# Performance work log

Measured on AMD Instinct MI355X. Metric: run time of the kernel, lower is better.

Reference implementation:

```python
import jax, jax.numpy as jnp
import numpy as np

# MSDeformAttn-style fusion config (canonical deformable-DETR defaults)
D = 256      # d_model
NH = 8       # n_heads
NP = 4       # n_points per level
NL = 2       # n_levels (= num_feature_levels: modality v and modality i)
B, H, W = 4, 64, 64


def setup_inputs() -> dict:
    key = jax.random.key(0)
    ks = jax.random.split(key, 8)
    s = 0.02
    return {
        'input_v': jax.random.normal(ks[0], (B, D, H, W), jnp.float32),
        'input_i': jax.random.normal(ks[1], (B, D, H, W), jnp.float32),
        'W_value': jax.random.normal(ks[2], (D, D), jnp.float32) * s,
        'b_value': jnp.zeros((D,), jnp.float32),
        'W_off':   jax.random.normal(ks[3], (D, NH * NL * NP * 2), jnp.float32) * s,
        'b_off':   jax.random.normal(ks[4], (NH * NL * NP * 2,), jnp.float32) * s,
        'W_attn':  jax.random.normal(ks[5], (D, NH * NL * NP), jnp.float32) * s,
        'b_attn':  jnp.zeros((NH * NL * NP,), jnp.float32),
        'W_out':   jax.random.normal(ks[6], (D, D), jnp.float32) * s,
        'b_out':   jnp.zeros((D,), jnp.float32),
    }


def _bilinear_sample(value_l, locs, Hl, Wl):
    # value_l: (B, NH, HW, dh)  flattened per-level value
    # locs:    (B, Lq, NH, NP, 2) normalized sampling locations in [0,1]
    # returns  (B, NH, Lq, NP, dh); grid_sample semantics: zeros padding, align_corners=False
    b, nh, hw, dh = value_l.shape
    lq = locs.shape[1]
    x = locs[..., 0] * Wl - 0.5
    y = locs[..., 1] * Hl - 0.5
    x0 = jnp.floor(x)
    y0 = jnp.floor(y)
    dx = x - x0
    dy = y - y0
    x0i = x0.astype(jnp.int32)
    y0i = y0.astype(jnp.int32)
    out = jnp.zeros((b, nh, lq, NP, dh), value_l.dtype)
    corners = [
        (x0i,     y0i,     (1 - dx) * (1 - dy)),
        (x0i + 1, y0i,     dx * (1 - dy)),
        (x0i,     y0i + 1, (1 - dx) * dy),
        (x0i + 1, y0i + 1, dx * dy),
    ]
    for xi, yi, wgt in corners:
        valid = ((xi >= 0) & (xi < Wl) & (yi >= 0) & (yi < Hl)).astype(value_l.dtype)
        idx = jnp.clip(yi, 0, Hl - 1) * Wl + jnp.clip(xi, 0, Wl - 1)      # (B,Lq,NH,NP)
        idx_t = idx.transpose(0, 2, 1, 3).reshape(b, nh, lq * NP, 1)       # (B,NH,Lq*NP,1)
        g = jnp.take_along_axis(value_l, idx_t, axis=2)                    # (B,NH,Lq*NP,dh)
        g = g.reshape(b, nh, lq, NP, dh)
        w_t = (wgt * valid).transpose(0, 2, 1, 3)[..., None]               # (B,NH,Lq,NP,1)
        out = out + g * w_t
    return out


def reference(input_v, input_i, W_value, b_value, W_off, b_off, W_attn, b_attn, W_out, b_out):
    b, c, h, w = input_v.shape
    hw = h * w
    lq = NL * hw
    dh = c // NH

    # flatten both modalities into one token sequence (level 0 = v, level 1 = i)
    src_v = input_v.reshape(b, c, hw).transpose(0, 2, 1)
    src_i = input_i.reshape(b, c, hw).transpose(0, 2, 1)
    src = jnp.concatenate([src_v, src_i], axis=1)                          # (B, Lq, C)

    value = (src @ W_value + b_value).reshape(b, lq, NH, dh)
    value = value.transpose(0, 2, 1, 3)                                    # (B, NH, Lq, dh)
    value_levels = [value[:, :, :hw], value[:, :, hw:]]

    offsets = (src @ W_off + b_off).reshape(b, lq, NH, NL, NP, 2)
    attn = jax.nn.softmax((src @ W_attn + b_attn).reshape(b, lq, NH, NL * NP), axis=-1)
    attn = attn.reshape(b, lq, NH, NL, NP)

    # reference points: normalized pixel centers, same grid for both levels
    xs = (jnp.arange(w, dtype=jnp.float32) + 0.5) / w
    ys = (jnp.arange(h, dtype=jnp.float32) + 0.5) / h
    gy, gx = jnp.meshgrid(ys, xs, indexing='ij')
    ref = jnp.stack([gx.reshape(-1), gy.reshape(-1)], axis=-1)             # (HW, 2)
    ref = jnp.concatenate([ref, ref], axis=0)                              # (Lq, 2)

    norm = jnp.array([w, h], dtype=jnp.float32)
    locs = ref[None, :, None, None, None, :] + offsets / norm              # (B,Lq,NH,NL,NP,2)

    sampled = jnp.stack(
        [_bilinear_sample(value_levels[l], locs[:, :, :, l], h, w) for l in range(NL)],
        axis=3)                                                            # (B,NH,Lq,NL,NP,dh)

    fused = jnp.einsum('bqhlp,bhqlpd->bqhd', attn, sampled).reshape(b, lq, c)
    out = fused @ W_out + b_out                                            # (B, Lq, C)

    out_v = out[:, :hw]
    out_i = out[:, hw:]
    o = out_v + out_i                                                      # (B, HW, C)
    return o.transpose(0, 2, 1).reshape(b, c, h, w)
```

## Files before the change

### kernel.cpp

```cpp
#include <hip/hip_runtime.h>

#define HW 4096
#define LQ 8192
#define DD 256

typedef __bf16 bf16x8 __attribute__((ext_vector_type(8)));
typedef float  f32x4  __attribute__((ext_vector_type(4)));
typedef unsigned int u32;
typedef u32 u32x4 __attribute__((ext_vector_type(4)));

#define GLOAD16(g, l) __builtin_amdgcn_global_load_lds(                     \
    (__attribute__((address_space(1))) void*)(g),                          \
    (__attribute__((address_space(3))) void*)(l), 16, 0, 0)

__global__ __launch_bounds__(256) void prep_src(const float* __restrict__ in_v,
                                                const float* __restrict__ in_i,
                                                char* __restrict__ srcS)
{
    __shared__ float tile[64][68];
    const int q0 = blockIdx.x * 64;
    const int k0 = blockIdx.y * 64;
    const int bz = blockIdx.z;
    const float* src = ((bz & 1) ? in_i : in_v) + (size_t)(bz >> 1) * (DD * HW);
    const int t  = threadIdx.x;
    const int ql = (t & 15) * 4;
    const int kl = t >> 4;
#pragma unroll
    for (int rr = 0; rr < 4; ++rr) {
        const float4 v = *(const float4*)(src + (size_t)(k0 + kl + rr * 16) * HW + q0 + ql);
        *(float4*)&tile[kl + rr * 16][ql] = v;
    }
    __syncthreads();
    const int qrow = t >> 2;
    const int kc   = (t & 3) * 16;
    const int row  = (bz >> 1) * LQ + (bz & 1) * HW + q0 + qrow;
    bf16x8 p0, p1;
#pragma unroll
    for (int j = 0; j < 8; ++j) {
        p0[j] = (__bf16)tile[kc + j][qrow];
        p1[j] = (__bf16)tile[kc + 8 + j][qrow];
    }
    char* drow = srcS + (size_t)row * 512;
    const int sw   = (row & 7) << 4;
    const int base = k0 * 2 + kc * 2;
    *(bf16x8*)(drow + ((base)      ^ sw)) = p0;
    *(bf16x8*)(drow + ((base + 16) ^ sw)) = p1;
}

__global__ __launch_bounds__(256) void prep_w(const float* __restrict__ Wv,
                                              const float* __restrict__ Wo,
                                              const float* __restrict__ Wa,
                                              const float* __restrict__ Wout,
                                              char* __restrict__ WcatT,
                                              char* __restrict__ WoutT)
{
    const int gi = blockIdx.x * 256 + threadIdx.x;
    if (gi < 448 * 32) {
        const int row = gi >> 5;
        const int g   = gi & 31;
        const int k   = g * 8;
        const float* col; int stride;
        if (row < 256)      { col = Wv + row;         stride = 256; }
        else if (row < 384) { col = Wo + (row - 256); stride = 128; }
        else                { col = Wa + (row - 384); stride = 64;  }
        bf16x8 p;
#pragma unroll
        for (int j = 0; j < 8; ++j) p[j] = (__bf16)col[(size_t)(k + j) * stride];
        char* d = WcatT + (size_t)row * 512;
        *(bf16x8*)(d + ((g * 16) ^ ((row & 7) << 4))) = p;
    } else {
        const int gj = gi - 448 * 32;
        if (gj >= 256 * 64) return;
        const int c = gj >> 6;
        const int g = gj & 63;
        const int k = (g * 8) & 255;
        bf16x8 p;
#pragma unroll
        for (int j = 0; j < 8; ++j) p[j] = (__bf16)Wout[(size_t)(k + j) * 256 + c];
        char* d = WoutT + (size_t)c * 1024;
        *(bf16x8*)(d + ((g * 16) ^ ((c & 7) << 4))) = p;
    }
}

__global__ __launch_bounds__(256) void mfma_proj(const char* __restrict__ srcS,
                                                 const char* __restrict__ WcatT,
                                                 const float* __restrict__ b_value,
                                                 const float* __restrict__ b_off,
                                                 const float* __restrict__ b_attn,
                                                 __bf16* __restrict__ valueB,
                                                 float* __restrict__ off,
                                                 float* __restrict__ attn)
{
    __shared__ char smem[24576];
    char* As = smem;
    char* Bs = smem + 16384;

    const int M0 = blockIdx.x * 128;
    const int N0 = blockIdx.y * 64;
    const int t = threadIdx.x;
    const int w = t >> 6;
    const int l = t & 63;
    const int lm = l & 15, lk = l >> 4;
    const int wave_m = (w >> 1) * 64;
    const int wave_n = (w & 1) * 32;

    f32x4 acc[4][2] = {};

    const char* Ab = As + (wave_m + lm) * 128;
    const char* Bb = Bs + (wave_n + lm) * 128;
    const int go0 = (lk ^ (l & 7)) * 16;
    const int go1 = go0 ^ 64;

    for (int kt = 0; kt < 4; ++kt) {
        __syncthreads();
        const int kb = kt * 128;
#pragma unroll
        for (int c = 0; c < 4; ++c) {
            const char* g = srcS + (size_t)(M0 + w * 32 + c * 8 + (l >> 3)) * 512 + kb + (l & 7) * 16;
            GLOAD16(g, As + (w * 4 + c) * 1024);
        }
#pragma unroll
        for (int c = 0; c < 2; ++c) {
            const char* g = WcatT + (size_t)(N0 + w * 16 + c * 8 + (l >> 3)) * 512 + kb + (l & 7) * 16;
            GLOAD16(g, Bs + (w * 2 + c) * 1024);
        }
        __syncthreads();

        bf16x8 af[4], bb[2];
#pragma unroll
        for (int mi = 0; mi < 4; ++mi) af[mi] = *(const bf16x8*)(Ab + mi * 2048 + go0);
#pragma unroll
        for (int ni = 0; ni < 2; ++ni) bb[ni] = *(const bf16x8*)(Bb + ni * 2048 + go0);
#pragma unroll
        for (int mi = 0; mi < 4; ++mi)
#pragma unroll
            for (int ni = 0; ni < 2; ++ni)
                acc[mi][ni] = __builtin_amdgcn_mfma_f32_16x16x32_bf16(af[mi], bb[ni], acc[mi][ni], 0, 0, 0);
#pragma unroll
        for (int mi = 0; mi < 4; ++mi) af[mi] = *(const bf16x8*)(Ab + mi * 2048 + go1);
#pragma unroll
        for (int ni = 0; ni < 2; ++ni) bb[ni] = *(const bf16x8*)(Bb + ni * 2048 + go1);
#pragma unroll
        for (int mi = 0; mi < 4; ++mi)
#pragma unroll
            for (int ni = 0; ni < 2; ++ni)
                acc[mi][ni] = __builtin_amdgcn_mfma_f32_16x16x32_bf16(af[mi], bb[ni], acc[mi][ni], 0, 0, 0);
    }

    if (N0 < 256) {
#pragma unroll
        for (int ni = 0; ni < 2; ++ni) {
            const int cl = N0 + wave_n + ni * 16 + lm;
            const float bv = b_value[cl];
#pragma unroll
            for (int mi = 0; mi < 4; ++mi) {
                const int row = M0 + wave_m + mi * 16 + lk * 4;
#pragma unroll
                for (int r = 0; r < 4; ++r)
                    valueB[(size_t)(row + r) * 256 + cl] = (__bf16)(acc[mi][ni][r] + bv);
            }
        }
    } else {
        float* outp; const float* bias; int ncols, nloc;
        if (N0 < 384) { outp = off;  bias = b_off;  ncols = 128; nloc = N0 - 256; }
        else          { outp = attn; bias = b_attn; ncols = 64;  nloc = N0 - 384; }
#pragma unroll
        for (int ni = 0; ni < 2; ++ni) {
            const int cl = nloc + wave_n + ni * 16 + lm;
            const float bv = bias[cl];
#pragma unroll
            for (int mi = 0; mi < 4; ++mi) {
                const int row = M0 + wave_m + mi * 16 + lk * 4;
#pragma unroll
                for (int r = 0; r < 4; ++r)
                    outp[(size_t)(row + r) * ncols + cl] = acc[mi][ni][r] + bv;
            }
        }
    }
}

__global__ __launch_bounds__(256) void sample_kernel(const char* __restrict__ valueB,
                                                     const float* __restrict__ offs,
                                                     const float* __restrict__ logits,
                                                     char* __restrict__ fusedS)
{
    const int wid  = (blockIdx.x << 2) + (threadIdx.x >> 6);
    const int lane = threadIdx.x & 63;
    const int q2   = lane >> 5;
    const int row  = wid * 2 + q2;
    const int sub  = lane & 31;
    const int head = sub >> 2;
    const int d8   = (sub & 3) << 3;
    const int b    = row >> 13;
    const int pix  = row & 4095;
    const float fx0 = (float)(pix & 63);
    const float fy0 = (float)(pix >> 6);

    const float* lg = logits + (size_t)row * 64 + head * 8;
    const float4 lgA = *(const float4*)lg;
    const float4 lgB = *(const float4*)(lg + 4);
    float e[8] = {lgA.x, lgA.y, lgA.z, lgA.w, lgB.x, lgB.y, lgB.z, lgB.w};
    float mx = e[0];
#pragma unroll
    for (int j = 1; j < 8; ++j) mx = fmaxf(mx, e[j]);
    float s = 0.f;
#pragma unroll
    for (int j = 0; j < 8; ++j) { e[j] = __expf(e[j] - mx); s += e[j]; }
    const float inv = 1.0f / s;

    const float* of = offs + (size_t)row * 128 + head * 16;
    float o[16];
#pragma unroll
    for (int j = 0; j < 4; ++j) {
        const float4 v4 = *(const float4*)(of + j * 4);
        o[j * 4 + 0] = v4.x; o[j * 4 + 1] = v4.y;
        o[j * 4 + 2] = v4.z; o[j * 4 + 3] = v4.w;
    }

    float acc[8] = {};
#pragma unroll
    for (int ll = 0; ll < 2; ++ll) {
        const char* vb = valueB + (((size_t)(b * LQ + ll * HW)) << 9) + head * 64 + d8 * 2;
#pragma unroll
        for (int p = 0; p < 4; ++p) {
            const float ox = o[ll * 8 + p * 2];
            const float oy = o[ll * 8 + p * 2 + 1];
            const float aw = e[ll * 4 + p] * inv;
            const float x = fx0 + ox;
            const float y = fy0 + oy;
            const float xf = floorf(x), yf = floorf(y);
            const int   xi = (int)xf,  yi = (int)yf;
            const float dx = x - xf,   dy = y - yf;
            float w00 = (1.f - dx) * (1.f - dy);
            float w10 = dx * (1.f - dy);
            float w01 = (1.f - dx) * dy;
            float w11 = dx * dy;
            const bool vx0 = (unsigned)xi       < 64u;
            const bool vx1 = (unsigned)(xi + 1) < 64u;
            const bool vy0 = (unsigned)yi       < 64u;
            const bool vy1 = (unsigned)(yi + 1) < 64u;
            const float u00 = (vx0 && vy0) ? aw * w00 : 0.f;
            const float u10 = (vx1 && vy0) ? aw * w10 : 0.f;
            const float u01 = (vx0 && vy1) ? aw * w01 : 0.f;
            const float u11 = (vx1 && vy1) ? aw * w11 : 0.f;
            const int xc0 = min(max(xi, 0), 63);
            const int xc1 = min(max(xi + 1, 0), 63);
            const int yc0 = min(max(yi, 0), 63) << 6;
            const int yc1 = min(max(yi + 1, 0), 63) << 6;
            const u32x4 g00 = *(const u32x4*)(vb + ((size_t)(yc0 + xc0) << 9));
            const u32x4 g10 = *(const u32x4*)(vb + ((size_t)(yc0 + xc1) << 9));
            const u32x4 g01 = *(const u32x4*)(vb + ((size_t)(yc1 + xc0) << 9));
            const u32x4 g11 = *(const u32x4*)(vb + ((size_t)(yc1 + xc1) << 9));
#pragma unroll
            for (int j = 0; j < 4; ++j) {
                const float l00 = __uint_as_float(g00[j] << 16);
                const float h00 = __uint_as_float(g00[j] & 0xffff0000u);
                const float l10 = __uint_as_float(g10[j] << 16);
                const float h10 = __uint_as_float(g10[j] & 0xffff0000u);
                const float l01 = __uint_as_float(g01[j] << 16);
                const float h01 = __uint_as_float(g01[j] & 0xffff0000u);
                const float l11 = __uint_as_float(g11[j] << 16);
                const float h11 = __uint_as_float(g11[j] & 0xffff0000u);
                acc[j * 2]     += u00 * l00 + u10 * l10 + u01 * l01 + u11 * l11;
                acc[j * 2 + 1] += u00 * h00 + u10 * h10 + u01 * h01 + u11 * h11;
            }
        }
    }
    bf16x8 ov;
#pragma unroll
    for (int j = 0; j < 8; ++j) ov[j] = (__bf16)acc[j];
    const int bo = (head * 64 + d8 * 2) ^ ((row & 7) << 4);
    *(bf16x8*)(fusedS + (size_t)row * 512 + bo) = ov;
}

__global__ __launch_bounds__(256) void mfma_out(const char* __restrict__ fusedS,
                                                const char* __restrict__ WoutT,
                                                const float* __restrict__ b_out,
                                                float* __restrict__ out)
{
    __shared__ char smem[24576];
    char* As = smem;
    char* Bs = smem + 16384;
    float* Tr = (float*)smem;

    const int M0 = blockIdx.x * 128;
    const int N0 = blockIdx.y * 64;
    const int bi = M0 >> 12;
    const int q0 = M0 & 4095;
    const int t = threadIdx.x;
    const int w = t >> 6;
    const int l = t & 63;
    const int lm = l & 15, lk = l >> 4;
    const int wave_m = (w >> 1) * 64;
    const int wave_n = (w & 1) * 32;

    f32x4 acc[4][2] = {};

    const char* Ab = As + (wave_m + lm) * 128;
    const char* Bb = Bs + (wave_n + lm) * 128;
    const int go0 = (lk ^ (l & 7)) * 16;
    const int go1 = go0 ^ 64;

    for (int kt = 0; kt < 8; ++kt) {
        __syncthreads();
        const int half = kt >> 2;
        const int kb   = (kt & 3) * 128;
#pragma unroll
        for (int c = 0; c < 4; ++c) {
            const char* g = fusedS + (size_t)(bi * LQ + half * HW + q0 + w * 32 + c * 8 + (l >> 3)) * 512
                          + kb + (l & 7) * 16;
            GLOAD16(g, As + (w * 4 + c) * 1024);
        }
#pragma unroll
        for (int c = 0; c < 2; ++c) {
            const char* g = WoutT + (size_t)(N0 + w * 16 + c * 8 + (l >> 3)) * 1024 + kt * 128 + (l & 7) * 16;
            GLOAD16(g, Bs + (w * 2 + c) * 1024);
        }
        __syncthreads();

        bf16x8 af[4], bb[2];
#pragma unroll
        for (int mi = 0; mi < 4; ++mi) af[mi] = *(const bf16x8*)(Ab + mi * 2048 + go0);
#pragma unroll
        for (int ni = 0; ni < 2; ++ni) bb[ni] = *(const bf16x8*)(Bb + ni * 2048 + go0);
#pragma unroll
        for (int mi = 0; mi < 4; ++mi)
#pragma unroll
            for (int ni = 0; ni < 2; ++ni)
                acc[mi][ni] = __builtin_amdgcn_mfma_f32_16x16x32_bf16(af[mi], bb[ni], acc[mi][ni], 0, 0, 0);
#pragma unroll
        for (int mi = 0; mi < 4; ++mi) af[mi] = *(const bf16x8*)(Ab + mi * 2048 + go1);
#pragma unroll
        for (int ni = 0; ni < 2; ++ni) bb[ni] = *(const bf16x8*)(Bb + ni * 2048 + go1);
#pragma unroll
        for (int mi = 0; mi < 4; ++mi)
#pragma unroll
            for (int ni = 0; ni < 2; ++ni)
                acc[mi][ni] = __builtin_amdgcn_mfma_f32_16x16x32_bf16(af[mi], bb[ni], acc[mi][ni], 0, 0, 0);
    }

    float bias2[2];
#pragma unroll
    for (int ni = 0; ni < 2; ++ni) bias2[ni] = 2.0f * b_out[N0 + wave_n + ni * 16 + lm];

#pragma unroll
    for (int h = 0; h < 2; ++h) {
        __syncthreads();
        if ((w >> 1) == h) {
#pragma unroll
            for (int mi = 0; mi < 4; ++mi)
#pragma unroll
                for (int ni = 0; ni < 2; ++ni)
#pragma unroll
                    for (int r = 0; r < 4; ++r)
                        Tr[(wave_n + ni * 16 + lm) * 68 + mi * 16 + lk * 4 + r] = acc[mi][ni][r] + bias2[ni];
        }
        __syncthreads();
        const int c  = t >> 2;
        const int qo = (t & 3) * 16;
        float* dst = out + ((size_t)(bi * DD + N0 + c)) * HW + q0 + h * 64 + qo;
        const float* sp = Tr + c * 68 + qo;
#pragma unroll
        for (int j = 0; j < 4; ++j)
            *(f32x4*)(dst + j * 4) = *(const f32x4*)(sp + j * 4);
    }
}

extern "C" void kernel_launch(void* const* d_in, const int* in_sizes, int n_in,
                              void* d_out, int out_size, void* d_ws, size_t ws_size,
                              hipStream_t stream) {
    const float* in_v    = (const float*)d_in[0];
    const float* in_i    = (const float*)d_in[1];
    const float* W_value = (const float*)d_in[2];
    const float* b_value = (const float*)d_in[3];
    const float* W_off   = (const float*)d_in[4];
    const float* b_off   = (const float*)d_in[5];
    const float* W_attn  = (const float*)d_in[6];
    const float* b_attn  = (const float*)d_in[7];
    const float* W_out   = (const float*)d_in[8];
    const float* b_out   = (const float*)d_in[9];
    float* out = (float*)d_out;

    char* ws = (char*)d_ws;
    __bf16* valueB = (__bf16*)(ws);
    float*  off_ws = (float*)(ws + 16777216);
    float*  attn_ws= (float*)(ws + 33554432);
    char*   srcS   = ws + 41943040;
    char*   fusedS = ws + 58720256;
    char*   WcatT  = ws + 75497472;
    char*   WoutT  = ws + 75726848;

    prep_src<<<dim3(64, 4, 8), 256, 0, stream>>>(in_v, in_i, srcS);
    prep_w<<<120, 256, 0, stream>>>(W_value, W_off, W_attn, W_out, WcatT, WoutT);
    mfma_proj<<<dim3(256, 7), 256, 0, stream>>>(srcS, WcatT, b_value, b_off, b_attn,
                                                valueB, off_ws, attn_ws);
    sample_kernel<<<dim3(4096), 256, 0, stream>>>((const char*)valueB, off_ws, attn_ws, fusedS);
    mfma_out<<<dim3(128, 4), 256, 0, stream>>>(fusedS, WoutT, b_out, out);
}
```

Measured before the change: 81.32 us.

## Merge prep kernels, store offsets/logits as bf16, tile sampling spatially with wider per-thread channels

Merges the source-transpose and weight-prep kernels into a single launch, using a ninth z-slice for the weight conversion. Offsets and attention logits are now stored in bf16, which halves their write and read traffic between the projection and sampling kernels. The sampling kernel now maps each wave to a 2x2-pixel spatial tile, inside 4x4 blocks, so neighbouring queries share gathered value rows in cache. Each thread handles 16 channels instead of 8, which halves the number of blocks. Storing offsets in bf16 loses precision in the sampling locations and may shift bilinear results.

New measurement: 100.6 us. +23.7%, slower.

```diff
diff --git a/kernel.cpp b/kernel.cpp
--- a/kernel.cpp
+++ b/kernel.cpp
@@ -9,76 +9,81 @@
 typedef unsigned int u32;
 typedef u32 u32x4 __attribute__((ext_vector_type(4)));
 
+__device__ __forceinline__ float bflo(u32 u) { return __uint_as_float(u << 16); }
+__device__ __forceinline__ float bfhi(u32 u) { return __uint_as_float(u & 0xffff0000u); }
+
 #define GLOAD16(g, l) __builtin_amdgcn_global_load_lds(                     \
     (__attribute__((address_space(1))) void*)(g),                          \
     (__attribute__((address_space(3))) void*)(l), 16, 0, 0)
 
-__global__ __launch_bounds__(256) void prep_src(const float* __restrict__ in_v,
+__global__ __launch_bounds__(256) void prep_all(const float* __restrict__ in_v,
                                                 const float* __restrict__ in_i,
-                                                char* __restrict__ srcS)
+                                                const float* __restrict__ Wv,
+                                                const float* __restrict__ Wo,
+                                                const float* __restrict__ Wa,
+                                                const float* __restrict__ Wout,
+                                                char* __restrict__ srcS,
+                                                char* __restrict__ WcatT,
+                                                char* __restrict__ WoutT)
 {
     __shared__ float tile[64][68];
-    const int q0 = blockIdx.x * 64;
-    const int k0 = blockIdx.y * 64;
-    const int bz = blockIdx.z;
-    const float* src = ((bz & 1) ? in_i : in_v) + (size_t)(bz >> 1) * (DD * HW);
-    const int t  = threadIdx.x;
-    const int ql = (t & 15) * 4;
-    const int kl = t >> 4;
-#pragma unroll
-    for (int rr = 0; rr < 4; ++rr) {
-        const float4 v = *(const float4*)(src + (size_t)(k0 + kl + rr * 16) * HW + q0 + ql);
-        *(float4*)&tile[kl + rr * 16][ql] = v;
-    }
-    __syncthreads();
-    const int qrow = t >> 2;
-    const int kc   = (t & 3) * 16;
-    const int row  = (bz >> 1) * LQ + (bz & 1) * HW + q0 + qrow;
-    bf16x8 p0, p1;
-#pragma unroll
-    for (int j = 0; j < 8; ++j) {
-        p0[j] = (__bf16)tile[kc + j][qrow];
-        p1[j] = (__bf16)tile[kc + 8 + j][qrow];
-    }
-    char* drow = srcS + (size_t)row * 512;
-    const int sw   = (row & 7) << 4;
-    const int base = k0 * 2 + kc * 2;
-    *(bf16x8*)(drow + ((base)      ^ sw)) = p0;
-    *(bf16x8*)(drow + ((base + 16) ^ sw)) = p1;
-}
-
-__global__ __launch_bounds__(256) void prep_w(const float* __restrict__ Wv,
-                                              const float* __restrict__ Wo,
-                                              const float* __restrict__ Wa,
-                                              const float* __restrict__ Wout,
-                                              char* __restrict__ WcatT,
-                                              char* __restrict__ WoutT)
-{
-    const int gi = blockIdx.x * 256 + threadIdx.x;
-    if (gi < 448 * 32) {
-        const int row = gi >> 5;
-        const int g   = gi & 31;
-        const int k   = g * 8;
-        const float* col; int stride;
-        if (row < 256)      { col = Wv + row;         stride = 256; }
-        else if (row < 384) { col = Wo + (row - 256); stride = 128; }
-        else                { col = Wa + (row - 384); stride = 64;  }
-        bf16x8 p;
-#pragma unroll
-        for (int j = 0; j < 8; ++j) p[j] = (__bf16)col[(size_t)(k + j) * stride];
-        char* d = WcatT + (size_t)row * 512;
-        *(bf16x8*)(d + ((g * 16) ^ ((row & 7) << 4))) = p;
+    if (blockIdx.z < 8) {
+        const int q0 = blockIdx.x * 64;
+        const int k0 = blockIdx.y * 64;
+        const int bz = blockIdx.z;
+        const float* src = ((bz & 1) ? in_i : in_v) + (size_t)(bz >> 1) * (DD * HW);
+        const int t  = threadIdx.x;
+        const int ql = (t & 15) * 4;
+        const int kl = t >> 4;
+#pragma unroll
+        for (int rr = 0; rr < 4; ++rr) {
+            const float4 v = *(const float4*)(src + (size_t)(k0 + kl + rr * 16) * HW + q0 + ql);
+            *(float4*)&tile[kl + rr * 16][ql] = v;
+        }
+        __syncthreads();
+        const int qrow = t >> 2;
+        const int kc   = (t & 3) * 16;
+        const int row  = (bz >> 1) * LQ + (bz & 1) * HW + q0 + qrow;
+        bf16x8 p0, p1;
+#pragma unroll
+        for (int j = 0; j < 8; ++j) {
+            p0[j] = (__bf16)tile[kc + j][qrow];
+            p1[j] = (__bf16)tile[kc + 8 + j][qrow];
+        }
+        char* drow = srcS + (size_t)row * 512;
+        const int sw   = (row & 7) << 4;
+        const int base = k0 * 2 + kc * 2;
+        *(bf16x8*)(drow + ((base)      ^ sw)) = p0;
+        *(bf16x8*)(drow + ((base + 16) ^ sw)) = p1;
     } else {
-        const int gj = gi - 448 * 32;
-        if (gj >= 256 * 64) return;
-        const int c = gj >> 6;
-        const int g = gj & 63;
-        const int k = (g * 8) & 255;
-        bf16x8 p;
-#pragma unroll
-        for (int j = 0; j < 8; ++j) p[j] = (__bf16)Wout[(size_t)(k + j) * 256 + c];
-        char* d = WoutT + (size_t)c * 1024;
-        *(bf16x8*)(d + ((g * 16) ^ ((c & 7) << 4))) = p;
+        const int flat = blockIdx.y * 64 + blockIdx.x;
+        if (flat >= 120) return;
+        const int gi = flat * 256 + threadIdx.x;
+        if (gi < 448 * 32) {
+            const int row = gi >> 5;
+            const int g   = gi & 31;
+            const int k   = g * 8;
+            const float* col; int stride;
+            if (row < 256)      { col = Wv + row;         stride = 256; }
+            else if (row < 384) { col = Wo + (row - 256); stride = 128; }
+            else                { col = Wa + (row - 384); stride = 64;  }
+            bf16x8 p;
+#pragma unroll
+            for (int j = 0; j < 8; ++j) p[j] = (__bf16)col[(size_t)(k + j) * stride];
+            char* d = WcatT + (size_t)row * 512;
+            *(bf16x8*)(d + ((g * 16) ^ ((row & 7) << 4))) = p;
+        } else {
+            const int gj = gi - 448 * 32;
+            if (gj >= 256 * 64) return;
+            const int c = gj >> 6;
+            const int g = gj & 63;
+            const int k = (g * 8) & 255;
+            bf16x8 p;
+#pragma unroll
+            for (int j = 0; j < 8; ++j) p[j] = (__bf16)Wout[(size_t)(k + j) * 256 + c];
+            char* d = WoutT + (size_t)c * 1024;
+            *(bf16x8*)(d + ((g * 16) ^ ((c & 7) << 4))) = p;
+        }
     }
 }
 
@@ -88,8 +93,8 @@
                                                  const float* __restrict__ b_off,
                                                  const float* __restrict__ b_attn,
                                                  __bf16* __restrict__ valueB,
-                                                 float* __restrict__ off,
-                                                 float* __restrict__ attn)
+                                                 __bf16* __restrict__ offB,
+                                                 __bf16* __restrict__ attnB)
 {
     __shared__ char smem[24576];
     char* As = smem;
@@ -160,46 +165,63 @@
                     valueB[(size_t)(row + r) * 256 + cl] = (__bf16)(acc[mi][ni][r] + bv);
             }
         }
-    } else {
-        float* outp; const float* bias; int ncols, nloc;
-        if (N0 < 384) { outp = off;  bias = b_off;  ncols = 128; nloc = N0 - 256; }
-        else          { outp = attn; bias = b_attn; ncols = 64;  nloc = N0 - 384; }
+    } else if (N0 < 384) {
 #pragma unroll
         for (int ni = 0; ni < 2; ++ni) {
-            const int cl = nloc + wave_n + ni * 16 + lm;
-            const float bv = bias[cl];
+            const int cl = (N0 - 256) + wave_n + ni * 16 + lm;
+            const float bv = b_off[cl];
 #pragma unroll
             for (int mi = 0; mi < 4; ++mi) {
                 const int row = M0 + wave_m + mi * 16 + lk * 4;
 #pragma unroll
                 for (int r = 0; r < 4; ++r)
-                    outp[(size_t)(row + r) * ncols + cl] = acc[mi][ni][r] + bv;
+                    offB[(size_t)(row + r) * 128 + cl] = (__bf16)(acc[mi][ni][r] + bv);
             }
         }
+    } else {
+#pragma unroll
+        for (int ni = 0; ni < 2; ++ni) {
+            const int cl = wave_n + ni * 16 + lm;
+            const float bv = b_attn[cl];
+#pragma unroll
+            for (int mi = 0; mi < 4; ++mi) {
+                const int row = M0 + wave_m + mi * 16 + lk * 4;
+#pragma unroll
+                for (int r = 0; r < 4; ++r)
+                    attnB[(size_t)(row + r) * 64 + cl] = (__bf16)(acc[mi][ni][r] + bv);
+            }
+        }
     }
 }
 
 __global__ __launch_bounds__(256) void sample_kernel(const char* __restrict__ valueB,
-                                                     const float* __restrict__ offs,
-                                                     const float* __restrict__ logits,
+                                                     const char* __restrict__ offB,
+                                                     const char* __restrict__ attnB,
                                                      char* __restrict__ fusedS)
 {
-    const int wid  = (blockIdx.x << 2) + (threadIdx.x >> 6);
+    const int bid  = blockIdx.x;
+    const int w    = threadIdx.x >> 6;
     const int lane = threadIdx.x & 63;
-    const int q2   = lane >> 5;
-    const int row  = wid * 2 + q2;
-    const int sub  = lane & 31;
-    const int head = sub >> 2;
-    const int d8   = (sub & 3) << 3;
-    const int b    = row >> 13;
-    const int pix  = row & 4095;
-    const float fx0 = (float)(pix & 63);
-    const float fy0 = (float)(pix >> 6);
-
-    const float* lg = logits + (size_t)row * 64 + head * 8;
-    const float4 lgA = *(const float4*)lg;
-    const float4 lgB = *(const float4*)(lg + 4);
-    float e[8] = {lgA.x, lgA.y, lgA.z, lgA.w, lgB.x, lgB.y, lgB.z, lgB.w};
+    const int qq   = lane >> 4;
+    const int sub  = lane & 15;
+    const int head = sub >> 1;
+    const int dl   = sub & 1;
+
+    const int px   = bid & 15;
+    const int py   = (bid >> 4) & 15;
+    const int half = (bid >> 8) & 1;
+    const int b    = bid >> 9;
+    const int x    = px * 4 + (w & 1) * 2 + (qq & 1);
+    const int y    = py * 4 + (w >> 1) * 2 + (qq >> 1);
+    const int pix  = y * 64 + x;
+    const int row  = b * LQ + half * HW + pix;
+    const float fx0 = (float)x;
+    const float fy0 = (float)y;
+
+    const u32x4 lgp = *(const u32x4*)(attnB + (size_t)row * 128 + head * 16);
+    float e[8];
+#pragma unroll
+    for (int j = 0; j < 4; ++j) { e[2 * j] = bflo(lgp[j]); e[2 * j + 1] = bfhi(lgp[j]); }
     float mx = e[0];
 #pragma unroll
     for (int j = 1; j < 8; ++j) mx = fmaxf(mx, e[j]);
@@ -208,29 +230,30 @@
     for (int j = 0; j < 8; ++j) { e[j] = __expf(e[j] - mx); s += e[j]; }
     const float inv = 1.0f / s;
 
-    const float* of = offs + (size_t)row * 128 + head * 16;
+    const char* ofp = offB + (size_t)row * 256 + head * 32;
+    const u32x4 o0 = *(const u32x4*)ofp;
+    const u32x4 o1 = *(const u32x4*)(ofp + 16);
     float o[16];
 #pragma unroll
     for (int j = 0; j < 4; ++j) {
-        const float4 v4 = *(const float4*)(of + j * 4);
-        o[j * 4 + 0] = v4.x; o[j * 4 + 1] = v4.y;
-        o[j * 4 + 2] = v4.z; o[j * 4 + 3] = v4.w;
-    }
-
-    float acc[8] = {};
+        o[2 * j]     = bflo(o0[j]); o[2 * j + 1] = bfhi(o0[j]);
+        o[8 + 2 * j] = bflo(o1[j]); o[9 + 2 * j] = bfhi(o1[j]);
+    }
+
+    float acc[16] = {};
 #pragma unroll
     for (int ll = 0; ll < 2; ++ll) {
-        const char* vb = valueB + (((size_t)(b * LQ + ll * HW)) << 9) + head * 64 + d8 * 2;
+        const char* vb = valueB + (((size_t)(b * LQ + ll * HW)) << 9) + head * 64 + dl * 32;
 #pragma unroll
         for (int p = 0; p < 4; ++p) {
             const float ox = o[ll * 8 + p * 2];
             const float oy = o[ll * 8 + p * 2 + 1];
             const float aw = e[ll * 4 + p] * inv;
-            const float x = fx0 + ox;
-            const float y = fy0 + oy;
-            const float xf = floorf(x), yf = floorf(y);
-            const int   xi = (int)xf,  yi = (int)yf;
-            const float dx = x - xf,   dy = y - yf;
+            const float xx = fx0 + ox;
+            const float yy = fy0 + oy;
+            const float xf = floorf(xx), yf = floorf(yy);
+            const int   xi = (int)xf,   yi = (int)yf;
+            const float dx = xx - xf,   dy = yy - yf;
             float w00 = (1.f - dx) * (1.f - dy);
             float w10 = dx * (1.f - dy);
             float w01 = (1.f - dx) * dy;
@@ -247,30 +270,31 @@
             const int xc1 = min(max(xi + 1, 0), 63);
             const int yc0 = min(max(yi, 0), 63) << 6;
             const int yc1 = min(max(yi + 1, 0), 63) << 6;
-            const u32x4 g00 = *(const u32x4*)(vb + ((size_t)(yc0 + xc0) << 9));
-            const u32x4 g10 = *(const u32x4*)(vb + ((size_t)(yc0 + xc1) << 9));
-            const u32x4 g01 = *(const u32x4*)(vb + ((size_t)(yc1 + xc0) << 9));
-            const u32x4 g11 = *(const u32x4*)(vb + ((size_t)(yc1 + xc1) << 9));
+            const char* c00 = vb + ((size_t)(yc0 + xc0) << 9);
+            const char* c10 = vb + ((size_t)(yc0 + xc1) << 9);
+            const char* c01 = vb + ((size_t)(yc1 + xc0) << 9);
+            const char* c11 = vb + ((size_t)(yc1 + xc1) << 9);
+            const u32x4 a00 = *(const u32x4*)c00, b00 = *(const u32x4*)(c00 + 16);
+            const u32x4 a10 = *(const u32x4*)c10, b10 = *(const u32x4*)(c10 + 16);
+            const u32x4 a01 = *(const u32x4*)c01, b01 = *(const u32x4*)(c01 + 16);
+            const u32x4 a11 = *(const u32x4*)c11, b11 = *(const u32x4*)(c11 + 16);
 #pragma unroll
             for (int j = 0; j < 4; ++j) {
-                const float l00 = __uint_as_float(g00[j] << 16);
-                const float h00 = __uint_as_float(g00[j] & 0xffff0000u);
-                const float l10 = __uint_as_float(g10[j] << 16);
-                const float h10 = __uint_as_float(g10[j] & 0xffff0000u);
-                const float l01 = __uint_as_float(g01[j] << 16);
-                const float h01 = __uint_as_float(g01[j] & 0xffff0000u);
-                const float l11 = __uint_as_float(g11[j] << 16);
-                const float h11 = __uint_as_float(g11[j] & 0xffff0000u);
-                acc[j * 2]     += u00 * l00 + u10 * l10 + u01 * l01 + u11 * l11;
-                acc[j * 2 + 1] += u00 * h00 + u10 * h10 + u01 * h01 + u11 * h11;
+                acc[2 * j]     += u00 * bflo(a00[j]) + u10 * bflo(a10[j]) + u01 * bflo(a01[j]) + u11 * bflo(a11[j]);
+                acc[2 * j + 1] += u00 * bfhi(a00[j]) + u10 * bfhi(a10[j]) + u01 * bfhi(a01[j]) + u11 * bfhi(a11[j]);
+                acc[8 + 2 * j] += u00 * bflo(b00[j]) + u10 * bflo(b10[j]) + u01 * bflo(b01[j]) + u11 * bflo(b11[j]);
+                acc[9 + 2 * j] += u00 * bfhi(b00[j]) + u10 * bfhi(b10[j]) + u01 * bfhi(b01[j]) + u11 * bfhi(b11[j]);
             }
         }
     }
-    bf16x8 ov;
-#pragma unroll
-    for (int j = 0; j < 8; ++j) ov[j] = (__bf16)acc[j];
-    const int bo = (head * 64 + d8 * 2) ^ ((row & 7) << 4);
-    *(bf16x8*)(fusedS + (size_t)row * 512 + bo) = ov;
+    bf16x8 ov0, ov1;
+#pragma unroll
+    for (int j = 0; j < 8; ++j) { ov0[j] = (__bf16)acc[j]; ov1[j] = (__bf16)acc[8 + j]; }
+    char* dr = fusedS + (size_t)row * 512;
+    const int sw   = (row & 7) << 4;
+    const int base = head * 64 + dl * 32;
+    *(bf16x8*)(dr + (base ^ sw))        = ov0;
+    *(bf16x8*)(dr + ((base + 16) ^ sw)) = ov1;
 }
 
 __global__ __launch_bounds__(256) void mfma_out(const char* __restrict__ fusedS,
@@ -383,17 +407,18 @@
 
     char* ws = (char*)d_ws;
     __bf16* valueB = (__bf16*)(ws);
-    float*  off_ws = (float*)(ws + 16777216);
-    float*  attn_ws= (float*)(ws + 33554432);
-    char*   srcS   = ws + 41943040;
-    char*   fusedS = ws + 58720256;
-    char*   WcatT  = ws + 75497472;
-    char*   WoutT  = ws + 75726848;
-
-    prep_src<<<dim3(64, 4, 8), 256, 0, stream>>>(in_v, in_i, srcS);
-    prep_w<<<120, 256, 0, stream>>>(W_value, W_off, W_attn, W_out, WcatT, WoutT);
+    __bf16* offB   = (__bf16*)(ws + 16777216);
+    __bf16* attnB  = (__bf16*)(ws + 25165824);
+    char*   srcS   = ws + 29360128;
+    char*   fusedS = ws + 46137344;
+    char*   WcatT  = ws + 62914560;
+    char*   WoutT  = ws + 63143936;
+
+    prep_all<<<dim3(64, 4, 9), 256, 0, stream>>>(in_v, in_i, W_value, W_off, W_attn, W_out,
+                                                 srcS, WcatT, WoutT);
     mfma_proj<<<dim3(256, 7), 256, 0, stream>>>(srcS, WcatT, b_value, b_off, b_attn,
-                                                valueB, off_ws, attn_ws);
-    sample_kernel<<<dim3(4096), 256, 0, stream>>>((const char*)valueB, off_ws, attn_ws, fusedS);
+                                                valueB, offB, attnB);
+    sample_kernel<<<dim3(2048), 256, 0, stream>>>((const char*)valueB, (const char*)offB,
+                                                  (const char*)attnB, fusedS);
     mfma_out<<<dim3(128, 4), 256, 0, stream>>>(fusedS, WoutT, b_out, out);
 }
```
